# Kernel tuning notes

Hardware: AMD Instinct MI355X
Metric: run time of the kernel (lower is better)

## Reference

```python
import jax, jax.numpy as jnp
import numpy as np

B, T, H = 2, 2048, 1024
NH = 16
HD = H // NH


def setup_inputs() -> dict:
    key = jax.random.key(0)
    ks = jax.random.split(key, 9)
    s = 0.02
    return {
        "x": jax.random.normal(ks[0], (B, T, H), dtype=jnp.float32),
        "attn_mask": jnp.ones((B, T), dtype=jnp.int32),
        "Wq": jax.random.normal(ks[1], (H, H), dtype=jnp.float32) * s,
        "bq": jnp.zeros((H,), dtype=jnp.float32),
        "Wk": jax.random.normal(ks[2], (H, H), dtype=jnp.float32) * s,
        "bk": jnp.zeros((H,), dtype=jnp.float32),
        "Wv": jax.random.normal(ks[3], (H, H), dtype=jnp.float32) * s,
        "bv": jnp.zeros((H,), dtype=jnp.float32),
        "Wo": jax.random.normal(ks[4], (H, H), dtype=jnp.float32) * s,
        "bo": jnp.zeros((H,), dtype=jnp.float32),
    }


def reference(x, attn_mask, Wq, bq, Wk, bk, Wv, bv, Wo, bo):
    Bc, Tc, Hc = x.shape
    scale = HD ** -0.5
    # projections; torch Linear: y = x @ W.T + b (here W stored as [in,out])
    q = (x @ Wq + bq).reshape(Bc, Tc, NH, HD).transpose(0, 2, 1, 3)  # [B,NH,T,HD]
    k = (x @ Wk + bk).reshape(Bc, Tc, NH, HD).transpose(0, 2, 1, 3)
    v = (x @ Wv + bv).reshape(Bc, Tc, NH, HD).transpose(0, 2, 1, 3)
    scores = jnp.einsum('bhqd,bhkd->bhqk', q, k) * scale  # [B,NH,T,T]
    mask = attn_mask.reshape(Bc, 1, 1, Tc)
    scores = jnp.where(mask == 0, jnp.float32(-jnp.inf), scores)
    probs = jax.nn.softmax(scores, axis=-1)
    ctx = jnp.einsum('bhqk,bhkd->bhqd', probs, v)  # [B,NH,T,HD]
    ctx = ctx.transpose(0, 2, 1, 3).reshape(Bc, Tc, Hc)
    out = ctx @ Wo + bo
    return out
```

## Files before the change

### kernel.cpp

```cpp
#include <hip/hip_runtime.h>

typedef _Float16 f16;
typedef _Float16 f16x8 __attribute__((ext_vector_type(8)));
typedef _Float16 f16x4 __attribute__((ext_vector_type(4)));
typedef __fp16 h16x2 __attribute__((ext_vector_type(2)));
typedef float f32x4 __attribute__((ext_vector_type(4)));

#define MFMA32(a, b, c) __builtin_amdgcn_mfma_f32_16x16x32_f16((a), (b), (c), 0, 0, 0)

static constexpr int Bb = 2, T = 2048, H = 1024, NH = 16, HD = 64;
static constexpr int M = Bb * T;
static constexpr int NQK = 2 * H;
#define QSCALE 0.1803368801111f

__device__ __forceinline__ void gload_lds16(const void* g, void* l) {
  __builtin_amdgcn_global_load_lds(
      (const __attribute__((address_space(1))) void*)g,
      (__attribute__((address_space(3))) void*)l, 16, 0, 0);
}

__global__ __launch_bounds__(256) void pack_all(const float* __restrict__ x,
                                                const float* __restrict__ Wq,
                                                const float* __restrict__ Wk,
                                                const float* __restrict__ Wv,
                                                const float* __restrict__ Wo,
                                                const float* __restrict__ bq,
                                                const float* __restrict__ bk,
                                                const float* __restrict__ bv,
                                                const int* __restrict__ mask,
                                                f16* __restrict__ xh,
                                                f16* __restrict__ WqkvT,
                                                f16* __restrict__ WoT,
                                                float* __restrict__ bqkv,
                                                float* __restrict__ maskf) {
  __shared__ f16 tile[64][65];
  const int bid = blockIdx.x;
  if (bid < 4096) {
    int i = bid * 256 + threadIdx.x;
    float4 v = ((const float4*)x)[i];
    f16x4 o;
    o[0] = (f16)v.x; o[1] = (f16)v.y; o[2] = (f16)v.z; o[3] = (f16)v.w;
    *(f16x4*)(xh + (size_t)i * 4) = o;
  } else if (bid < 5120) {
    int t = bid - 4096;
    int z = t >> 8, rem = t & 255;
    const float* W = (z == 0) ? Wq : (z == 1) ? Wk : (z == 2) ? Wv : Wo;
    f16* Wt = (z < 3) ? (WqkvT + (size_t)z * H * H) : WoT;
    const float scale = (z == 0) ? QSCALE : 1.0f;
    int k0 = (rem >> 4) * 64, n0 = (rem & 15) * 64;
    for (int p = 0; p < 16; ++p) {
      int idx = threadIdx.x + p * 256;
      int r = idx >> 6, c = idx & 63;
      tile[r][c] = (f16)(W[(size_t)(k0 + r) * H + n0 + c] * scale);
    }
    __syncthreads();
    for (int p = 0; p < 16; ++p) {
      int idx = threadIdx.x + p * 256;
      int r = idx >> 6, c = idx & 63;
      Wt[(size_t)(n0 + r) * H + k0 + c] = tile[c][r];
    }
  } else if (bid < 5132) {
    int i = (bid - 5120) * 256 + threadIdx.x;
    if (i < 3072) {
      float v = (i < 1024) ? bq[i] * QSCALE : ((i < 2048) ? bk[i - 1024] : bv[i - 2048]);
      bqkv[i] = v;
    }
  } else {
    int i = (bid - 5132) * 256 + threadIdx.x;
    if (i < Bb * T) maskf[i] = mask[i] ? 0.0f : -30000.0f;
  }
}

__device__ __forceinline__ f16x8 lds_frag(const f16* base, int row, int gr) {
  return *(const f16x8*)(base + row * 64 + ((gr ^ (row & 7)) << 3));
}

__global__ __launch_bounds__(256, 3) void gemm_qkv(const f16* __restrict__ A,
                                                   const f16* __restrict__ Bt,
                                                   const float* __restrict__ bias,
                                                   f16* __restrict__ QK,
                                                   f16* __restrict__ VT) {
  constexpr int TM = 128, TN = 64, Kk = 1024;
  __shared__ f16 As[2][TM * 64];
  __shared__ f16 Bs[2][TN * 64];
  const int tid = threadIdx.x;
  const int lane = tid & 63, w = tid >> 6;
  const int quad = lane >> 4, l16 = lane & 15;
  const int wm = w >> 1, wn = w & 1;
  const int m0 = blockIdx.y * TM, n0 = blockIdx.x * TN;

  f32x4 acc[4][2];
  for (int a = 0; a < 4; ++a)
    for (int b2 = 0; b2 < 2; ++b2)
      for (int r = 0; r < 4; ++r) acc[a][b2][r] = 0.f;

  auto stage = [&](int k0, int buf) {
    for (int p = 0; p < 4; ++p) {
      int slot = p * 256 + w * 64 + lane;
      int r = slot >> 3, g = (slot & 7) ^ (r & 7);
      gload_lds16(A + (size_t)(m0 + r) * Kk + k0 + g * 8,
                  (char*)&As[buf][0] + (p * 256 + w * 64) * 16);
    }
    for (int p = 0; p < 2; ++p) {
      int slot = p * 256 + w * 64 + lane;
      int r = slot >> 3, g = (slot & 7) ^ (r & 7);
      gload_lds16(Bt + (size_t)(n0 + r) * Kk + k0 + g * 8,
                  (char*)&Bs[buf][0] + (p * 256 + w * 64) * 16);
    }
  };

  stage(0, 0);
  __syncthreads();
  for (int it = 0; it < Kk / 64; ++it) {
    const int cur = it & 1;
    if (it + 1 < Kk / 64) stage((it + 1) * 64, cur ^ 1);
    for (int ks = 0; ks < 2; ++ks) {
      f16x8 af[4], bf[2];
      for (int t = 0; t < 4; ++t)
        af[t] = lds_frag(&As[cur][0], wm * 64 + t * 16 + l16, ks * 4 + quad);
      for (int t = 0; t < 2; ++t)
        bf[t] = lds_frag(&Bs[cur][0], wn * 32 + t * 16 + l16, ks * 4 + quad);
      for (int tm = 0; tm < 4; ++tm)
        for (int tn = 0; tn < 2; ++tn)
          acc[tm][tn] = MFMA32(af[tm], bf[tn], acc[tm][tn]);
    }
    __syncthreads();
  }

  if (n0 < 2048) {
    for (int tm = 0; tm < 4; ++tm)
      for (int tn = 0; tn < 2; ++tn) {
        int n = n0 + wn * 32 + tn * 16 + l16;
        float bn = bias[n];
        for (int r = 0; r < 4; ++r) {
          int m = m0 + wm * 64 + tm * 16 + quad * 4 + r;
          QK[(size_t)m * NQK + n] = (f16)(acc[tm][tn][r] + bn);
        }
      }
  } else {
    for (int tm = 0; tm < 4; ++tm)
      for (int tn = 0; tn < 2; ++tn) {
        int ng = n0 + wn * 32 + tn * 16 + l16;
        float bn = bias[ng];
        int n = ng - 2048;
        int h = n >> 6, d = n & 63;
        int mrow = m0 + wm * 64 + tm * 16 + quad * 4;
        int bb = mrow >> 11, t = mrow & 2047;
        int c = (t & ~127) | ((t + 8 * (d & 15)) & 127);
        f16x4 o;
        for (int r = 0; r < 4; ++r) o[r] = (f16)(acc[tm][tn][r] + bn);
        *(f16x4*)(VT + ((size_t)(bb * NH + h) * HD + d) * T + c) = o;
      }
  }
}

__global__ __launch_bounds__(256, 3) void gemm_out(const f16* __restrict__ A,
                                                   const f16* __restrict__ Bt,
                                                   const float* __restrict__ bias,
                                                   float* __restrict__ Cout) {
  constexpr int TM = 128, TN = 64, Kk = 1024, Nn = 1024;
  __shared__ f16 As[2][TM * 64];
  __shared__ f16 Bs[2][TN * 64];
  const int tid = threadIdx.x;
  const int lane = tid & 63, w = tid >> 6;
  const int quad = lane >> 4, l16 = lane & 15;
  const int wm = w >> 1, wn = w & 1;
  const int m0 = blockIdx.y * TM, n0 = blockIdx.x * TN;

  f32x4 acc[4][2];
  for (int a = 0; a < 4; ++a)
    for (int b2 = 0; b2 < 2; ++b2)
      for (int r = 0; r < 4; ++r) acc[a][b2][r] = 0.f;

  auto stage = [&](int k0, int buf) {
    for (int p = 0; p < 4; ++p) {
      int slot = p * 256 + w * 64 + lane;
      int r = slot >> 3, g = (slot & 7) ^ (r & 7);
      gload_lds16(A + (size_t)(m0 + r) * Kk + k0 + g * 8,
                  (char*)&As[buf][0] + (p * 256 + w * 64) * 16);
    }
    for (int p = 0; p < 2; ++p) {
      int slot = p * 256 + w * 64 + lane;
      int r = slot >> 3, g = (slot & 7) ^ (r & 7);
      gload_lds16(Bt + (size_t)(n0 + r) * Kk + k0 + g * 8,
                  (char*)&Bs[buf][0] + (p * 256 + w * 64) * 16);
    }
  };

  stage(0, 0);
  __syncthreads();
  for (int it = 0; it < Kk / 64; ++it) {
    const int cur = it & 1;
    if (it + 1 < Kk / 64) stage((it + 1) * 64, cur ^ 1);
    for (int ks = 0; ks < 2; ++ks) {
      f16x8 af[4], bf[2];
      for (int t = 0; t < 4; ++t)
        af[t] = lds_frag(&As[cur][0], wm * 64 + t * 16 + l16, ks * 4 + quad);
      for (int t = 0; t < 2; ++t)
        bf[t] = lds_frag(&Bs[cur][0], wn * 32 + t * 16 + l16, ks * 4 + quad);
      for (int tm = 0; tm < 4; ++tm)
        for (int tn = 0; tn < 2; ++tn)
          acc[tm][tn] = MFMA32(af[tm], bf[tn], acc[tm][tn]);
    }
    __syncthreads();
  }

  for (int tm = 0; tm < 4; ++tm)
    for (int tn = 0; tn < 2; ++tn) {
      int n = n0 + wn * 32 + tn * 16 + l16;
      float bn = bias[n];
      for (int r = 0; r < 4; ++r) {
        int m = m0 + wm * 64 + tm * 16 + quad * 4 + r;
        Cout[(size_t)m * Nn + n] = acc[tm][tn][r] + bn;
      }
    }
}


static constexpr int KT_ELE = 128 * 64;
static constexpr int VT_ELE = 64 * 128;

__global__ __launch_bounds__(512, 2) void attn_fused(const f16* __restrict__ QK,
                                                     const f16* __restrict__ VT,
                                                     const float* __restrict__ maskf,
                                                     f16* __restrict__ ctx) {
  __shared__ __align__(16) char smem[70656];
  f16* KtB = (f16*)smem;
  f16* VtB = (f16*)(smem + 2 * KT_ELE * 2);

  const int tid = threadIdx.x;
  const int w = tid >> 6, lane = tid & 63;
  const int quad = lane >> 4, l16 = lane & 15;
  const int qw = w & 3, g = w >> 2;

  const int flat = blockIdx.x + (T / 256) * (blockIdx.y + NH * blockIdx.z);
  const int xcd = flat & 7, idx = flat >> 3;
  const int bh = xcd * 4 + (idx >> 3);
  const int qb = idx & 7;
  const int h = bh & 15, b = bh >> 4;
  const int q0 = qb * 256;

  const size_t kbase = (size_t)(b * T) * NQK + H + h * HD;
  const size_t vtbase = ((size_t)(b * NH + h) * HD) * T;
  const float* maskp = maskf + b * T;

  f16x8 qf[4][2];
  for (int tq = 0; tq < 4; ++tq) {
    const f16* qrow = QK + (size_t)(b * T + q0 + qw * 64 + tq * 16 + l16) * NQK + h * HD;
    qf[tq][0] = *(const f16x8*)(qrow + quad * 8);
    qf[tq][1] = *(const f16x8*)(qrow + 32 + quad * 8);
  }

  f16x8 onesf;
  for (int i = 0; i < 8; ++i) onesf[i] = (f16)1.0f;

  f32x4 oacc[4][4];
  f32x4 lacc[4];
  for (int tq = 0; tq < 4; ++tq) {
    for (int r = 0; r < 4; ++r) lacc[tq][r] = 0.f;
    for (int t = 0; t < 4; ++t)
      for (int r = 0; r < 4; ++r) oacc[tq][t][r] = 0.f;
  }

  auto stage = [&](int kv0, int buf) {
    f16* Kd = KtB + buf * KT_ELE;
    f16* Vd = VtB + buf * VT_ELE;
    for (int p = 0; p < 2; ++p) {
      int s = p * 512 + tid;
      int R = s >> 3, sg = (s & 7) ^ (R & 7);
      int kv = (R & ~31) | ((R & 12) << 1) | ((R & 16) >> 2) | (R & 3);
      gload_lds16(QK + kbase + (size_t)(kv0 + kv) * NQK + sg * 8,
                  (char*)Kd + (p * 512 + w * 64) * 16);
    }
    for (int p = 0; p < 2; ++p) {
      int s = p * 512 + tid;
      int d = s >> 4, cg = s & 15;
      gload_lds16(VT + vtbase + (size_t)d * T + kv0 + cg * 8,
                  (char*)Vd + (p * 512 + w * 64) * 16);
    }
  };

  stage(0, 0);
  __syncthreads();

  for (int it = 0; it < T / 128; ++it) {
    const int cur = it & 1;
    if (it + 1 < T / 128) stage((it + 1) * 128, cur ^ 1);

    const f16* Kc = KtB + cur * KT_ELE;
    const f16* Vc = VtB + cur * VT_ELE;

    for (int s = 0; s < 2; ++s) {
      const int bi = g * 2 + s;
      const int kvabs = it * 128 + bi * 32;
      float4 m0 = *(const float4*)(maskp + kvabs + quad * 8);
      float4 m1 = *(const float4*)(maskp + kvabs + quad * 8 + 4);
      f32x4 zA, zB;
      zA[0] = m0.x; zA[1] = m0.y; zA[2] = m0.z; zA[3] = m0.w;
      zB[0] = m1.x; zB[1] = m1.y; zB[2] = m1.z; zB[3] = m1.w;
      f16x8 kfA0 = lds_frag(Kc, bi * 32 + l16, quad);
      f16x8 kfA1 = lds_frag(Kc, bi * 32 + l16, 4 + quad);
      f16x8 kfB0 = lds_frag(Kc, bi * 32 + 16 + l16, quad);
      f16x8 kfB1 = lds_frag(Kc, bi * 32 + 16 + l16, 4 + quad);
      f16x8 vf[4];
      for (int td = 0; td < 4; ++td)
        vf[td] = *(const f16x8*)&Vc[(td * 16 + l16) * 128 +
                                    ((bi * 32 + quad * 8 + 8 * l16) & 127)];

      f32x4 sA[4], sB[4];
      for (int tq = 0; tq < 4; ++tq) {
        sA[tq] = MFMA32(kfA0, qf[tq][0], zA);
        sB[tq] = MFMA32(kfB0, qf[tq][0], zB);
      }
      for (int tq = 0; tq < 4; ++tq) {
        sA[tq] = MFMA32(kfA1, qf[tq][1], sA[tq]);
        sB[tq] = MFMA32(kfB1, qf[tq][1], sB[tq]);
      }

      f16x8 pf[4];
      for (int tq = 0; tq < 4; ++tq) {
        float pA0 = __builtin_amdgcn_exp2f(sA[tq][0]);
        float pA1 = __builtin_amdgcn_exp2f(sA[tq][1]);
        float pA2 = __builtin_amdgcn_exp2f(sA[tq][2]);
        float pA3 = __builtin_amdgcn_exp2f(sA[tq][3]);
        float pB0 = __builtin_amdgcn_exp2f(sB[tq][0]);
        float pB1 = __builtin_amdgcn_exp2f(sB[tq][1]);
        float pB2 = __builtin_amdgcn_exp2f(sB[tq][2]);
        float pB3 = __builtin_amdgcn_exp2f(sB[tq][3]);
        union PF { f16x8 v; h16x2 h[4]; } u;
        u.h[0] = __builtin_amdgcn_cvt_pkrtz(pA0, pA1);
        u.h[1] = __builtin_amdgcn_cvt_pkrtz(pA2, pA3);
        u.h[2] = __builtin_amdgcn_cvt_pkrtz(pB0, pB1);
        u.h[3] = __builtin_amdgcn_cvt_pkrtz(pB2, pB3);
        pf[tq] = u.v;
      }

      for (int tq = 0; tq < 4; ++tq) {
        for (int td = 0; td < 4; ++td)
          oacc[tq][td] = MFMA32(vf[td], pf[tq], oacc[tq][td]);
        lacc[tq] = MFMA32(onesf, pf[tq], lacc[tq]);
      }
    }
    __syncthreads();
  }

  float* cmb = (float*)smem;
  const int slot = qw * 64 + lane;
  if (g == 1) {
    float* dst = cmb + slot * 69;
    int i = 0;
    for (int tq = 0; tq < 4; ++tq)
      for (int td = 0; td < 4; ++td)
        for (int r = 0; r < 4; ++r) dst[i++] = oacc[tq][td][r];
    for (int tq = 0; tq < 4; ++tq) dst[64 + tq] = lacc[tq][0];
  }
  __syncthreads();
  if (g == 0) {
    const float* src = cmb + slot * 69;
    int i = 0;
    for (int tq = 0; tq < 4; ++tq)
      for (int td = 0; td < 4; ++td)
        for (int r = 0; r < 4; ++r) oacc[tq][td][r] += src[i++];

    for (int tq = 0; tq < 4; ++tq) {
      float l = lacc[tq][0] + src[64 + tq];
      float inv = 1.f / l;
      int row = b * T + q0 + qw * 64 + tq * 16 + l16;
      for (int td = 0; td < 4; ++td) {
        f16x4 o;
        for (int r = 0; r < 4; ++r) o[r] = (f16)(oacc[tq][td][r] * inv);
        *(f16x4*)(ctx + (size_t)row * H + h * HD + td * 16 + quad * 4) = o;
      }
    }
  }
}


extern "C" void kernel_launch(void* const* d_in, const int* in_sizes, int n_in,
                              void* d_out, int out_size, void* d_ws, size_t ws_size,
                              hipStream_t stream) {
  const float* x  = (const float*)d_in[0];
  const int* mask = (const int*)d_in[1];
  const float* Wq = (const float*)d_in[2];
  const float* bq = (const float*)d_in[3];
  const float* Wk = (const float*)d_in[4];
  const float* bk = (const float*)d_in[5];
  const float* Wv = (const float*)d_in[6];
  const float* bv = (const float*)d_in[7];
  const float* Wo = (const float*)d_in[8];
  const float* bo = (const float*)d_in[9];
  float* out = (float*)d_out;

  char* ws = (char*)d_ws;
  f16* xh      = (f16*)(ws);
  f16* Wqkv_t  = (f16*)(ws + (8u  << 20));
  f16* Wot     = (f16*)(ws + (14u << 20));
  float* bqkv  = (float*)(ws + (16u << 20));
  float* maskf = (float*)(ws + (16u << 20) + 65536);
  f16* QK      = (f16*)(ws + (17u << 20));
  f16* ctx     = (f16*)(ws + (34u << 20));
  f16* VTr     = (f16*)(ws + (43u << 20));

  pack_all<<<dim3(5164), 256, 0, stream>>>(x, Wq, Wk, Wv, Wo, bq, bk, bv, mask,
                                           xh, Wqkv_t, Wot, bqkv, maskf);

  gemm_qkv<<<dim3(3 * H / 64, M / 128), 256, 0, stream>>>(
      xh, Wqkv_t, bqkv, QK, VTr);

  attn_fused<<<dim3(T / 256, NH, Bb), 512, 0, stream>>>(QK, VTr, maskf, ctx);

  gemm_out<<<dim3(H / 64, M / 128), 256, 0, stream>>>(ctx, Wot, bo, out);
}
```

Before: 184.6 us.

## Triple-buffer attention KV loads, stage mask in LDS, swizzle GEMM block order

The attention kernel moves from double to triple buffering of K/V tiles. It uses explicit vmcnt waits and raw s_barrier so one tile stays in flight while another is consumed, and it preloads the mask row into LDS instead of reading it from global memory each step. MFMA sections are wrapped in s_setprio to favour matrix issue. Both GEMM kernels remap block indices so neighbouring tiles land on the same XCD for better L2 reuse. LDS grows to about 104KB, which may limit two blocks per CU, and the hand-written waitcnt logic is fragile.

```diff
diff --git a/kernel.cpp b/kernel.cpp
--- a/kernel.cpp
+++ b/kernel.cpp
@@ -87,7 +87,12 @@
   const int lane = tid & 63, w = tid >> 6;
   const int quad = lane >> 4, l16 = lane & 15;
   const int wm = w >> 1, wn = w & 1;
-  const int m0 = blockIdx.y * TM, n0 = blockIdx.x * TN;
+
+  const int flat = blockIdx.y * 48 + blockIdx.x;
+  const int xq = flat & 7, xr = flat >> 3;
+  const int bx = (xq & 1) * 24 + (xr % 24);
+  const int by = (xq >> 1) * 8 + (xr / 24);
+  const int m0 = by * TM, n0 = bx * TN;
 
   f32x4 acc[4][2];
   for (int a = 0; a < 4; ++a)
@@ -165,7 +170,12 @@
   const int lane = tid & 63, w = tid >> 6;
   const int quad = lane >> 4, l16 = lane & 15;
   const int wm = w >> 1, wn = w & 1;
-  const int m0 = blockIdx.y * TM, n0 = blockIdx.x * TN;
+
+  const int flat = blockIdx.y * 16 + blockIdx.x;
+  const int xq = flat & 7, xr = flat >> 3;
+  const int bx = (xq & 1) * 8 + (xr % 8);
+  const int by = (xq >> 1) * 8 + (xr / 8);
+  const int m0 = by * TM, n0 = bx * TN;
 
   f32x4 acc[4][2];
   for (int a = 0; a < 4; ++a)
@@ -219,14 +229,15 @@
 
 static constexpr int KT_ELE = 128 * 64;
 static constexpr int VT_ELE = 64 * 128;
+static constexpr int BUF_B = 32768;
+static constexpr int NT = T / 128;
 
 __global__ __launch_bounds__(512, 2) void attn_fused(const f16* __restrict__ QK,
                                                      const f16* __restrict__ VT,
                                                      const float* __restrict__ maskf,
                                                      f16* __restrict__ ctx) {
-  __shared__ __align__(16) char smem[70656];
-  f16* KtB = (f16*)smem;
-  f16* VtB = (f16*)(smem + 2 * KT_ELE * 2);
+  __shared__ __align__(16) char smem[106496];
+  float* maskLds = (float*)(smem + 3 * BUF_B);
 
   const int tid = threadIdx.x;
   const int w = tid >> 6, lane = tid & 63;
@@ -263,38 +274,41 @@
   }
 
   auto stage = [&](int kv0, int buf) {
-    f16* Kd = KtB + buf * KT_ELE;
-    f16* Vd = VtB + buf * VT_ELE;
+    char* Kd = smem + buf * BUF_B;
+    char* Vd = Kd + KT_ELE * 2;
     for (int p = 0; p < 2; ++p) {
       int s = p * 512 + tid;
       int R = s >> 3, sg = (s & 7) ^ (R & 7);
       int kv = (R & ~31) | ((R & 12) << 1) | ((R & 16) >> 2) | (R & 3);
       gload_lds16(QK + kbase + (size_t)(kv0 + kv) * NQK + sg * 8,
-                  (char*)Kd + (p * 512 + w * 64) * 16);
+                  Kd + (p * 512 + w * 64) * 16);
     }
     for (int p = 0; p < 2; ++p) {
       int s = p * 512 + tid;
       int d = s >> 4, cg = s & 15;
       gload_lds16(VT + vtbase + (size_t)d * T + kv0 + cg * 8,
-                  (char*)Vd + (p * 512 + w * 64) * 16);
+                  Vd + (p * 512 + w * 64) * 16);
     }
   };
 
+  gload_lds16(maskp + tid * 4, (char*)maskLds + tid * 16);
+
   stage(0, 0);
-  __syncthreads();
-
-  for (int it = 0; it < T / 128; ++it) {
-    const int cur = it & 1;
-    if (it + 1 < T / 128) stage((it + 1) * 128, cur ^ 1);
-
-    const f16* Kc = KtB + cur * KT_ELE;
-    const f16* Vc = VtB + cur * VT_ELE;
+  stage(128, 1);
+  asm volatile("s_waitcnt vmcnt(4)" ::: "memory");
+  __builtin_amdgcn_sched_barrier(0);
+  __builtin_amdgcn_s_barrier();
+
+  for (int it = 0; it < NT; ++it) {
+    const f16* Kc = (const f16*)(smem + (it % 3) * BUF_B);
+    const f16* Vc = (const f16*)(smem + (it % 3) * BUF_B + KT_ELE * 2);
+    if (it + 2 < NT) stage((it + 2) * 128, (it + 2) % 3);
 
     for (int s = 0; s < 2; ++s) {
       const int bi = g * 2 + s;
       const int kvabs = it * 128 + bi * 32;
-      float4 m0 = *(const float4*)(maskp + kvabs + quad * 8);
-      float4 m1 = *(const float4*)(maskp + kvabs + quad * 8 + 4);
+      float4 m0 = *(const float4*)&maskLds[kvabs + quad * 8];
+      float4 m1 = *(const float4*)&maskLds[kvabs + quad * 8 + 4];
       f32x4 zA, zB;
       zA[0] = m0.x; zA[1] = m0.y; zA[2] = m0.z; zA[3] = m0.w;
       zB[0] = m1.x; zB[1] = m1.y; zB[2] = m1.z; zB[3] = m1.w;
@@ -308,6 +322,7 @@
                                     ((bi * 32 + quad * 8 + 8 * l16) & 127)];
 
       f32x4 sA[4], sB[4];
+      __builtin_amdgcn_s_setprio(1);
       for (int tq = 0; tq < 4; ++tq) {
         sA[tq] = MFMA32(kfA0, qf[tq][0], zA);
         sB[tq] = MFMA32(kfB0, qf[tq][0], zB);
@@ -316,6 +331,7 @@
         sA[tq] = MFMA32(kfA1, qf[tq][1], sA[tq]);
         sB[tq] = MFMA32(kfB1, qf[tq][1], sB[tq]);
       }
+      __builtin_amdgcn_s_setprio(0);
 
       f16x8 pf[4];
       for (int tq = 0; tq < 4; ++tq) {
@@ -335,14 +351,27 @@
         pf[tq] = u.v;
       }
 
+      __builtin_amdgcn_s_setprio(1);
       for (int tq = 0; tq < 4; ++tq) {
         for (int td = 0; td < 4; ++td)
           oacc[tq][td] = MFMA32(vf[td], pf[tq], oacc[tq][td]);
         lacc[tq] = MFMA32(onesf, pf[tq], lacc[tq]);
       }
-    }
-    __syncthreads();
-  }
+      __builtin_amdgcn_s_setprio(0);
+    }
+
+    if (it + 2 < NT) {
+      asm volatile("s_waitcnt vmcnt(4)" ::: "memory");
+      __builtin_amdgcn_sched_barrier(0);
+      __builtin_amdgcn_s_barrier();
+    } else if (it + 1 < NT) {
+      asm volatile("s_waitcnt vmcnt(0)" ::: "memory");
+      __builtin_amdgcn_sched_barrier(0);
+      __builtin_amdgcn_s_barrier();
+    }
+  }
+
+  __syncthreads();
 
   float* cmb = (float*)smem;
   const int slot = qw * 64 + lane;
```

New measurement: 189.9 us. +2.9%, slower.
